# Kernel tuning notes

Measured on AMD Instinct MI355X. Metric: run time of the kernel, lower is better.

The kernel has to match this reference:

```python
import jax, jax.numpy as jnp
import numpy as np

NUM_STAGES = 8
NUM_CODEBOOKS = 1024  # 2**10
DATA_DIM = 256
T = 131072


def setup_inputs() -> dict:
    key = jax.random.key(0)
    k_x, k_cb = jax.random.split(key)
    input_data = jax.random.normal(k_x, (T, DATA_DIM), dtype=jnp.float32)
    # torch init: Uniform(-1/K, 1/K) per stage
    bound = 1.0 / NUM_CODEBOOKS
    codebooks = jax.random.uniform(
        k_cb, (NUM_STAGES, NUM_CODEBOOKS, DATA_DIM), dtype=jnp.float32,
        minval=-bound, maxval=bound)
    return {"input_data": input_data, "codebooks": codebooks}


def _hard_vq(residual, cb):
    dists = (jnp.sum(residual * residual, axis=1, keepdims=True)
             - 2.0 * (residual @ cb.T)
             + jnp.sum(cb * cb, axis=1)[None, :])
    idx = jnp.argmin(dists, axis=1)          # [T]
    q = cb[idx]                               # gather -> [T, D]
    return q, residual - q, idx


def reference(input_data, codebooks):
    # eval path: stage_map=None (mask of ones), train_mode=False
    residual = input_data
    recon = jnp.zeros_like(input_data)
    mses = []
    for i in range(codebooks.shape[0]):  # fixed small stage loop
        q, residual, _ = _hard_vq(residual, codebooks[i])
        recon = recon + q  # intermediate reconstruction = cumulative sum of q
        mses.append(jnp.mean((recon - input_data) ** 2))
    final_output = recon
    return final_output, jnp.stack(mses)
```

## Files before the change

kernel.cpp:

```cpp
#include <hip/hip_runtime.h>
#include <stdint.h>


#define T_ROWS   131072
#define DIM      256
#define NSTAGE   8
#define NCB      1024
#define WROWS    32
#define NWAVE    8
#define BLK_ROWS (NWAVE * WROWS)
#define NTHREADS (NWAVE * 64)
#define CHUNK_CW 32
#define NCHUNK   (NCB / CHUNK_CW)
#define CHUNK_BYTES (CHUNK_CW * 512)
#define NBUF     4

#define WS_CB_BYTES    (NSTAGE * NCB * 512)
#define WS_CNORM_OFF   WS_CB_BYTES
#define WS_CNORM_BYTES (NSTAGE * NCB * 4)
#define WS_MSE_OFF     (WS_CNORM_OFF + WS_CNORM_BYTES)
#define WS_IDX_OFF     (WS_MSE_OFF + 64)

typedef __attribute__((ext_vector_type(8)))  short  s16x8;
typedef __attribute__((ext_vector_type(8)))  __bf16 bf16x8;
typedef __attribute__((ext_vector_type(4)))  float  f32x4;
typedef __attribute__((ext_vector_type(16))) float  f32x16;

__device__ __forceinline__ unsigned short f2bf(float f) {
  union { float f; unsigned u; } v; v.f = f;
  unsigned r = v.u + 0x7FFFu + ((v.u >> 16) & 1u);
  return (unsigned short)(r >> 16);
}

__global__ void vq_prep(const float* __restrict__ CB, char* __restrict__ wscb,
                        float* __restrict__ cnorm) {
  const int tid = threadIdx.x;
  const int cwl = tid >> 5;
  const int j   = tid & 31;
  const int cw  = blockIdx.x * 8 + cwl;
  const int c   = cw & (NCB - 1);
  const float* src = CB + (size_t)cw * DIM + 8 * j;
  f32x4 a = *(const f32x4*)(src);
  f32x4 b = *(const f32x4*)(src + 4);
  s16x8 h;
#pragma unroll
  for (int e = 0; e < 4; ++e) { h[e] = (short)f2bf(a[e]); h[4 + e] = (short)f2bf(b[e]); }
  float sq = a[0]*a[0] + a[1]*a[1] + a[2]*a[2] + a[3]*a[3]
           + b[0]*b[0] + b[1]*b[1] + b[2]*b[2] + b[3]*b[3];
#pragma unroll
  for (int m = 1; m <= 16; m <<= 1) sq += __shfl_xor(sq, m);
  *(s16x8*)(wscb + (size_t)cw * 512 + ((16 * j) ^ ((c & 31) << 4))) = h;
  if (j == 0) cnorm[cw] = sq;
}

__global__ __launch_bounds__(NTHREADS, 4)
void vq_search(const float* __restrict__ X,
               const char* __restrict__ wscb, const float* __restrict__ cnorm,
               unsigned short* __restrict__ IDX, float* __restrict__ wsmse) {
  __shared__ __align__(16) char  lds_cb[NBUF][CHUNK_BYTES];
  __shared__ __align__(16) float lds_cn[NCB];
  __shared__ unsigned short lds_idx[BLK_ROWS];
  __shared__ float lds_n[BLK_ROWS];
  __shared__ float lds_msum[NWAVE];

  const int tid  = threadIdx.x;
  const int wave = tid >> 6;
  const int lane = tid & 63;
  const int c32  = lane & 31;
  const int hi   = lane >> 5;

  const int rowbase = blockIdx.x * BLK_ROWS + wave * WROWS;

  bf16x8 af[16];
  {
    const float* px = X + (size_t)(rowbase + c32) * DIM + 8 * hi;
    float s2 = 0.f;
#pragma unroll
    for (int s = 0; s < 16; ++s) {
      f32x4 a = *(const f32x4*)(px + 16 * s);
      f32x4 b = *(const f32x4*)(px + 16 * s + 4);
      bf16x8 tt;
#pragma unroll
      for (int e = 0; e < 4; ++e) {
        tt[e] = (__bf16)a[e]; tt[4 + e] = (__bf16)b[e];
        s2 += a[e] * a[e] + b[e] * b[e];
      }
      af[s] = tt;
    }
    float v = s2 + __shfl_xor(s2, 32);
    if (lane < 32) lds_n[wave * WROWS + c32] = v;
  }

  if (wave < 4)
    __builtin_amdgcn_global_load_lds(
        (const __attribute__((address_space(1))) char*)((const char*)cnorm + wave * 1024 + lane * 16),
        (__attribute__((address_space(3))) char*)((char*)lds_cn + wave * 1024),
        16, 0, 0);
#pragma unroll
  for (int ch = 0; ch < 3; ++ch)
#pragma unroll
    for (int i = 0; i < 2; ++i) {
      const int seg = (wave * 2 + i) * 1024;
      __builtin_amdgcn_global_load_lds(
          (const __attribute__((address_space(1))) char*)(wscb + (size_t)ch * CHUNK_BYTES + seg + lane * 16),
          (__attribute__((address_space(3))) char*)(&lds_cb[ch][0] + seg),
          16, 0, 0);
    }

  const int swz = c32 << 4;

#pragma unroll 1
  for (int st = 0; st < NSTAGE; ++st) {
    float mv[16];
#pragma unroll
    for (int r = 0; r < 16; ++r) mv[r] = -3.402823466e38f;

    const char* stage_cb = wscb + (size_t)st * NCB * 512;

#pragma unroll 1
    for (int ch = 0; ch < NCHUNK; ++ch) {
      const int cur = ch & (NBUF - 1);

      if (ch < NCHUNK - 2) {
        asm volatile("s_waitcnt vmcnt(4)" ::: "memory");
      } else if (ch == NCHUNK - 2) {
        asm volatile("s_waitcnt vmcnt(2)" ::: "memory");
      } else {
        asm volatile("s_waitcnt vmcnt(0)" ::: "memory");
      }
      __builtin_amdgcn_sched_barrier(0);
      __builtin_amdgcn_s_barrier();
      __builtin_amdgcn_sched_barrier(0);

      const float cnv = lds_cn[ch * CHUNK_CW + c32];
      f32x16 acc;
#pragma unroll
      for (int r = 0; r < 16; ++r) acc[r] = 0.f;

      const char* buf = &lds_cb[cur][0];
      __builtin_amdgcn_s_setprio(1);
#pragma unroll
      for (int s = 0; s < 16; ++s) {
        bf16x8 b = *(const bf16x8*)(buf + c32 * 512 + ((s * 32 + hi * 16) ^ swz));
        acc = __builtin_amdgcn_mfma_f32_32x32x16_bf16(af[s], b, acc, 0, 0, 0);
      }
      __builtin_amdgcn_s_setprio(0);

      if (ch + 3 < NCHUNK) {
        const char* src = stage_cb + (size_t)(ch + 3) * CHUNK_BYTES;
        char* dst = &lds_cb[(ch + 3) & (NBUF - 1)][0];
#pragma unroll
        for (int i = 0; i < 2; ++i) {
          const int seg = (wave * 2 + i) * 1024;
          __builtin_amdgcn_global_load_lds(
              (const __attribute__((address_space(1))) char*)(src + seg + lane * 16),
              (__attribute__((address_space(3))) char*)(dst + seg),
              16, 0, 0);
        }
      }

      const float cnh = 0.5f * cnv;
      const unsigned col = (unsigned)(ch * CHUNK_CW + c32);
#pragma unroll
      for (int r = 0; r < 16; ++r) {
        union { float f; unsigned u; } p;
        p.f = acc[r] - cnh;
        p.u = (p.u & 0xFFFFFC00u) | col;
        mv[r] = fmaxf(mv[r], p.f);
      }
    }

    float msum = 0.f;
#pragma unroll
    for (int r = 0; r < 16; ++r) {
      float v = mv[r];
#pragma unroll
      for (int m = 1; m <= 16; m <<= 1) v = fmaxf(v, __shfl_xor(v, m));
      union { float f; unsigned u; } w; w.f = v;
      const float vtrue = __builtin_bit_cast(float, w.u & 0xFFFFFC00u);
      const int   row   = (r & 3) + 8 * (r >> 2) + 4 * hi;
      const int   wrow  = wave * WROWS + row;
      const float n_new = lds_n[wrow] - 2.0f * vtrue;
      msum += n_new;
      if (c32 == 0) {
        lds_n[wrow]   = n_new;
        const int ix = (int)(w.u & 1023u);
        lds_idx[wrow] = (unsigned short)ix;
        IDX[st * T_ROWS + rowbase + row] = (unsigned short)ix;
      }
    }
    msum += __shfl_xor(msum, 32);
    if (lane == 0) lds_msum[wave] = msum;

    if (st != NSTAGE - 1) {
      const int idx = (int)lds_idx[wave * WROWS + c32];
      const char* q = stage_cb + (size_t)idx * 512;
      const int swzu = (idx & 31) << 4;
#pragma unroll
      for (int s = 0; s < 16; ++s) {
        bf16x8 qb = *(const bf16x8*)(q + ((s * 32 + hi * 16) ^ swzu));
        bf16x8 tt = af[s];
#pragma unroll
        for (int e = 0; e < 8; ++e)
          tt[e] = (__bf16)((float)tt[e] - (float)qb[e]);
        af[s] = tt;
      }
    }

    __builtin_amdgcn_sched_barrier(0);
    __builtin_amdgcn_s_barrier();
    __builtin_amdgcn_sched_barrier(0);

    if (wave == 0) {
      float v = (lane < NWAVE) ? lds_msum[lane] : 0.f;
#pragma unroll
      for (int m = 1; m < NWAVE; m <<= 1) v += __shfl_xor(v, m);
      if (lane == 0) atomicAdd(wsmse + st, v);
    }

    if (st != NSTAGE - 1) {
      const char* ncb = stage_cb + (size_t)NCB * 512;
      const char* ncn = (const char*)cnorm + (size_t)(st + 1) * NCB * 4;
      if (wave < 4)
        __builtin_amdgcn_global_load_lds(
            (const __attribute__((address_space(1))) char*)(ncn + wave * 1024 + lane * 16),
            (__attribute__((address_space(3))) char*)((char*)lds_cn + wave * 1024),
            16, 0, 0);
#pragma unroll
      for (int ch = 0; ch < 3; ++ch)
#pragma unroll
        for (int i = 0; i < 2; ++i) {
          const int seg = (wave * 2 + i) * 1024;
          __builtin_amdgcn_global_load_lds(
              (const __attribute__((address_space(1))) char*)(ncb + (size_t)ch * CHUNK_BYTES + seg + lane * 16),
              (__attribute__((address_space(3))) char*)(&lds_cb[ch][0] + seg),
              16, 0, 0);
        }
    }
  }
}

__global__ __launch_bounds__(256)
void vq_recon(const char* __restrict__ wscb, const unsigned short* __restrict__ IDX,
              float* __restrict__ OUT) {
  const int tid = threadIdx.x;
  const int row = blockIdx.x * (256 / 8) + (tid >> 3);
  const int g   = tid & 7;

  int idxs[NSTAGE];
#pragma unroll
  for (int st = 0; st < NSTAGE; ++st) idxs[st] = IDX[st * T_ROWS + row];

  float a[32];
#pragma unroll
  for (int d = 0; d < 32; ++d) a[d] = 0.f;

#pragma unroll
  for (int st = 0; st < NSTAGE; ++st) {
    const char* q = wscb + ((size_t)st * NCB + idxs[st]) * 512;
    const int swzu = (idxs[st] & 31) << 4;
#pragma unroll
    for (int k = 0; k < 4; ++k) {
      bf16x8 qb = *(const bf16x8*)(q + ((g * 64 + 16 * k) ^ swzu));
#pragma unroll
      for (int e = 0; e < 8; ++e) a[k * 8 + e] += (float)qb[e];
    }
  }

  float* po = OUT + (size_t)row * DIM + g * 32;
#pragma unroll
  for (int m = 0; m < 8; ++m) {
    f32x4 o = {a[4 * m], a[4 * m + 1], a[4 * m + 2], a[4 * m + 3]};
    *(f32x4*)(po + 4 * m) = o;
  }
}

__global__ void vq_fin(const float* __restrict__ wsmse, float* __restrict__ OUT) {
  const int i = threadIdx.x;
  if (i < NSTAGE) {
    OUT[(size_t)T_ROWS * DIM + i] = wsmse[i] * (1.0f / ((float)T_ROWS * (float)DIM));
  }
}

extern "C" void kernel_launch(void* const* d_in, const int* in_sizes, int n_in,
                              void* d_out, int out_size, void* d_ws, size_t ws_size,
                              hipStream_t stream) {
  (void)in_sizes; (void)n_in; (void)out_size; (void)ws_size;
  const float* X  = (const float*)d_in[0];
  const float* CB = (const float*)d_in[1];
  float* OUT = (float*)d_out;
  char*  wscb  = (char*)d_ws;
  float* cnorm = (float*)((char*)d_ws + WS_CNORM_OFF);
  float* wsmse = (float*)((char*)d_ws + WS_MSE_OFF);
  unsigned short* IDX = (unsigned short*)((char*)d_ws + WS_IDX_OFF);

  hipMemsetAsync(wsmse, 0, NSTAGE * sizeof(float), stream);
  hipLaunchKernelGGL(vq_prep, dim3((NSTAGE * NCB) / 8), dim3(256), 0, stream,
                     CB, wscb, cnorm);
  hipLaunchKernelGGL(vq_search, dim3(T_ROWS / BLK_ROWS), dim3(NTHREADS), 0, stream,
                     X, wscb, cnorm, IDX, wsmse);
  hipLaunchKernelGGL(vq_recon, dim3(T_ROWS / (256 / 8)), dim3(256), 0, stream,
                     wscb, IDX, OUT);
  hipLaunchKernelGGL(vq_fin, dim3(1), dim3(64), 0, stream, wsmse, OUT);
}
```

Baseline: 700.8 us.

## Give each wave four row tiles to reuse codebook LDS fragments across MFMAs

Each wave now processes 128 rows as four 32-row tiles with 4 waves per block, so each codebook fragment read from LDS feeds four MFMAs instead of one. This cuts LDS read traffic per MFMA and software-prefetches the next B fragment. It costs far more registers (four A tile sets, four accumulators and four max arrays), so launch bounds drop to one block per SM. Codebook streaming is now spread across fewer waves with more loads each, and fewer waves are available to hide latency.

```diff
diff --git a/kernel.cpp b/kernel.cpp
--- a/kernel.cpp
+++ b/kernel.cpp
@@ -6,8 +6,9 @@
 #define DIM      256
 #define NSTAGE   8
 #define NCB      1024
-#define WROWS    32
-#define NWAVE    8
+#define WROWS    128
+#define NTILE    4
+#define NWAVE    4
 #define BLK_ROWS (NWAVE * WROWS)
 #define NTHREADS (NWAVE * 64)
 #define CHUNK_CW 32
@@ -53,7 +54,7 @@
   if (j == 0) cnorm[cw] = sq;
 }
 
-__global__ __launch_bounds__(NTHREADS, 4)
+__global__ __launch_bounds__(NTHREADS, 1)
 void vq_search(const float* __restrict__ X,
                const char* __restrict__ wscb, const float* __restrict__ cnorm,
                unsigned short* __restrict__ IDX, float* __restrict__ wsmse) {
@@ -71,9 +72,10 @@
 
   const int rowbase = blockIdx.x * BLK_ROWS + wave * WROWS;
 
-  bf16x8 af[16];
-  {
-    const float* px = X + (size_t)(rowbase + c32) * DIM + 8 * hi;
+  bf16x8 af[NTILE][16];
+#pragma unroll
+  for (int t = 0; t < NTILE; ++t) {
+    const float* px = X + (size_t)(rowbase + t * 32 + c32) * DIM + 8 * hi;
     float s2 = 0.f;
 #pragma unroll
     for (int s = 0; s < 16; ++s) {
@@ -85,22 +87,21 @@
         tt[e] = (__bf16)a[e]; tt[4 + e] = (__bf16)b[e];
         s2 += a[e] * a[e] + b[e] * b[e];
       }
-      af[s] = tt;
+      af[t][s] = tt;
     }
     float v = s2 + __shfl_xor(s2, 32);
-    if (lane < 32) lds_n[wave * WROWS + c32] = v;
-  }
-
-  if (wave < 4)
-    __builtin_amdgcn_global_load_lds(
-        (const __attribute__((address_space(1))) char*)((const char*)cnorm + wave * 1024 + lane * 16),
-        (__attribute__((address_space(3))) char*)((char*)lds_cn + wave * 1024),
-        16, 0, 0);
+    if (lane < 32) lds_n[wave * WROWS + t * 32 + c32] = v;
+  }
+
+  __builtin_amdgcn_global_load_lds(
+      (const __attribute__((address_space(1))) char*)((const char*)cnorm + wave * 1024 + lane * 16),
+      (__attribute__((address_space(3))) char*)((char*)lds_cn + wave * 1024),
+      16, 0, 0);
 #pragma unroll
   for (int ch = 0; ch < 3; ++ch)
 #pragma unroll
-    for (int i = 0; i < 2; ++i) {
-      const int seg = (wave * 2 + i) * 1024;
+    for (int i = 0; i < 4; ++i) {
+      const int seg = (wave * 4 + i) * 1024;
       __builtin_amdgcn_global_load_lds(
           (const __attribute__((address_space(1))) char*)(wscb + (size_t)ch * CHUNK_BYTES + seg + lane * 16),
           (__attribute__((address_space(3))) char*)(&lds_cb[ch][0] + seg),
@@ -111,9 +112,11 @@
 
 #pragma unroll 1
   for (int st = 0; st < NSTAGE; ++st) {
-    float mv[16];
-#pragma unroll
-    for (int r = 0; r < 16; ++r) mv[r] = -3.402823466e38f;
+    float mv[NTILE][16];
+#pragma unroll
+    for (int t = 0; t < NTILE; ++t)
+#pragma unroll
+      for (int r = 0; r < 16; ++r) mv[t][r] = -3.402823466e38f;
 
     const char* stage_cb = wscb + (size_t)st * NCB * 512;
 
@@ -122,9 +125,9 @@
       const int cur = ch & (NBUF - 1);
 
       if (ch < NCHUNK - 2) {
+        asm volatile("s_waitcnt vmcnt(8)" ::: "memory");
+      } else if (ch == NCHUNK - 2) {
         asm volatile("s_waitcnt vmcnt(4)" ::: "memory");
-      } else if (ch == NCHUNK - 2) {
-        asm volatile("s_waitcnt vmcnt(2)" ::: "memory");
       } else {
         asm volatile("s_waitcnt vmcnt(0)" ::: "memory");
       }
@@ -133,16 +136,22 @@
       __builtin_amdgcn_sched_barrier(0);
 
       const float cnv = lds_cn[ch * CHUNK_CW + c32];
-      f32x16 acc;
-#pragma unroll
-      for (int r = 0; r < 16; ++r) acc[r] = 0.f;
-
-      const char* buf = &lds_cb[cur][0];
+      f32x16 acc0, acc1, acc2, acc3;
+#pragma unroll
+      for (int r = 0; r < 16; ++r) { acc0[r] = 0.f; acc1[r] = 0.f; acc2[r] = 0.f; acc3[r] = 0.f; }
+
+      const char* base = &lds_cb[cur][0] + c32 * 512;
       __builtin_amdgcn_s_setprio(1);
+      bf16x8 bcur = *(const bf16x8*)(base + ((hi * 16) ^ swz));
 #pragma unroll
       for (int s = 0; s < 16; ++s) {
-        bf16x8 b = *(const bf16x8*)(buf + c32 * 512 + ((s * 32 + hi * 16) ^ swz));
-        acc = __builtin_amdgcn_mfma_f32_32x32x16_bf16(af[s], b, acc, 0, 0, 0);
+        bf16x8 bnext;
+        if (s < 15) bnext = *(const bf16x8*)(base + (((s + 1) * 32 + hi * 16) ^ swz));
+        acc0 = __builtin_amdgcn_mfma_f32_32x32x16_bf16(af[0][s], bcur, acc0, 0, 0, 0);
+        acc1 = __builtin_amdgcn_mfma_f32_32x32x16_bf16(af[1][s], bcur, acc1, 0, 0, 0);
+        acc2 = __builtin_amdgcn_mfma_f32_32x32x16_bf16(af[2][s], bcur, acc2, 0, 0, 0);
+        acc3 = __builtin_amdgcn_mfma_f32_32x32x16_bf16(af[3][s], bcur, acc3, 0, 0, 0);
+        if (s < 15) bcur = bnext;
       }
       __builtin_amdgcn_s_setprio(0);
 
@@ -150,8 +159,8 @@
         const char* src = stage_cb + (size_t)(ch + 3) * CHUNK_BYTES;
         char* dst = &lds_cb[(ch + 3) & (NBUF - 1)][0];
 #pragma unroll
-        for (int i = 0; i < 2; ++i) {
-          const int seg = (wave * 2 + i) * 1024;
+        for (int i = 0; i < 4; ++i) {
+          const int seg = (wave * 4 + i) * 1024;
           __builtin_amdgcn_global_load_lds(
               (const __attribute__((address_space(1))) char*)(src + seg + lane * 16),
               (__attribute__((address_space(3))) char*)(dst + seg),
@@ -163,47 +172,57 @@
       const unsigned col = (unsigned)(ch * CHUNK_CW + c32);
 #pragma unroll
       for (int r = 0; r < 16; ++r) {
-        union { float f; unsigned u; } p;
-        p.f = acc[r] - cnh;
-        p.u = (p.u & 0xFFFFFC00u) | col;
-        mv[r] = fmaxf(mv[r], p.f);
+        union { float f; unsigned u; } p0, p1, p2, p3;
+        p0.f = acc0[r] - cnh; p0.u = (p0.u & 0xFFFFFC00u) | col;
+        p1.f = acc1[r] - cnh; p1.u = (p1.u & 0xFFFFFC00u) | col;
+        p2.f = acc2[r] - cnh; p2.u = (p2.u & 0xFFFFFC00u) | col;
+        p3.f = acc3[r] - cnh; p3.u = (p3.u & 0xFFFFFC00u) | col;
+        mv[0][r] = fmaxf(mv[0][r], p0.f);
+        mv[1][r] = fmaxf(mv[1][r], p1.f);
+        mv[2][r] = fmaxf(mv[2][r], p2.f);
+        mv[3][r] = fmaxf(mv[3][r], p3.f);
       }
     }
 
     float msum = 0.f;
 #pragma unroll
-    for (int r = 0; r < 16; ++r) {
-      float v = mv[r];
-#pragma unroll
-      for (int m = 1; m <= 16; m <<= 1) v = fmaxf(v, __shfl_xor(v, m));
-      union { float f; unsigned u; } w; w.f = v;
-      const float vtrue = __builtin_bit_cast(float, w.u & 0xFFFFFC00u);
-      const int   row   = (r & 3) + 8 * (r >> 2) + 4 * hi;
-      const int   wrow  = wave * WROWS + row;
-      const float n_new = lds_n[wrow] - 2.0f * vtrue;
-      msum += n_new;
-      if (c32 == 0) {
-        lds_n[wrow]   = n_new;
-        const int ix = (int)(w.u & 1023u);
-        lds_idx[wrow] = (unsigned short)ix;
-        IDX[st * T_ROWS + rowbase + row] = (unsigned short)ix;
-      }
-    }
+    for (int t = 0; t < NTILE; ++t)
+#pragma unroll
+      for (int r = 0; r < 16; ++r) {
+        float v = mv[t][r];
+#pragma unroll
+        for (int m = 1; m <= 16; m <<= 1) v = fmaxf(v, __shfl_xor(v, m));
+        union { float f; unsigned u; } w; w.f = v;
+        const float vtrue = __builtin_bit_cast(float, w.u & 0xFFFFFC00u);
+        const int   row   = t * 32 + (r & 3) + 8 * (r >> 2) + 4 * hi;
+        const int   wrow  = wave * WROWS + row;
+        const float n_new = lds_n[wrow] - 2.0f * vtrue;
+        msum += n_new;
+        if (c32 == 0) {
+          lds_n[wrow]   = n_new;
+          const int ix = (int)(w.u & 1023u);
+          lds_idx[wrow] = (unsigned short)ix;
+          IDX[st * T_ROWS + rowbase + row] = (unsigned short)ix;
+        }
+      }
     msum += __shfl_xor(msum, 32);
     if (lane == 0) lds_msum[wave] = msum;
 
     if (st != NSTAGE - 1) {
-      const int idx = (int)lds_idx[wave * WROWS + c32];
-      const char* q = stage_cb + (size_t)idx * 512;
-      const int swzu = (idx & 31) << 4;
-#pragma unroll
-      for (int s = 0; s < 16; ++s) {
-        bf16x8 qb = *(const bf16x8*)(q + ((s * 32 + hi * 16) ^ swzu));
-        bf16x8 tt = af[s];
-#pragma unroll
-        for (int e = 0; e < 8; ++e)
-          tt[e] = (__bf16)((float)tt[e] - (float)qb[e]);
-        af[s] = tt;
+#pragma unroll
+      for (int t = 0; t < NTILE; ++t) {
+        const int idx = (int)lds_idx[wave * WROWS + t * 32 + c32];
+        const char* q = stage_cb + (size_t)idx * 512;
+        const int swzu = (idx & 31) << 4;
+#pragma unroll
+        for (int s = 0; s < 16; ++s) {
+          bf16x8 qb = *(const bf16x8*)(q + ((s * 32 + hi * 16) ^ swzu));
+          bf16x8 tt = af[t][s];
+#pragma unroll
+          for (int e = 0; e < 8; ++e)
+            tt[e] = (__bf16)((float)tt[e] - (float)qb[e]);
+          af[t][s] = tt;
+        }
       }
     }
 
@@ -213,24 +232,23 @@
 
     if (wave == 0) {
       float v = (lane < NWAVE) ? lds_msum[lane] : 0.f;
-#pragma unroll
-      for (int m = 1; m < NWAVE; m <<= 1) v += __shfl_xor(v, m);
+      v += __shfl_xor(v, 1);
+      v += __shfl_xor(v, 2);
       if (lane == 0) atomicAdd(wsmse + st, v);
     }
 
     if (st != NSTAGE - 1) {
       const char* ncb = stage_cb + (size_t)NCB * 512;
       const char* ncn = (const char*)cnorm + (size_t)(st + 1) * NCB * 4;
-      if (wave < 4)
-        __builtin_amdgcn_global_load_lds(
-            (const __attribute__((address_space(1))) char*)(ncn + wave * 1024 + lane * 16),
-            (__attribute__((address_space(3))) char*)((char*)lds_cn + wave * 1024),
-            16, 0, 0);
+      __builtin_amdgcn_global_load_lds(
+          (const __attribute__((address_space(1))) char*)(ncn + wave * 1024 + lane * 16),
+          (__attribute__((address_space(3))) char*)((char*)lds_cn + wave * 1024),
+          16, 0, 0);
 #pragma unroll
       for (int ch = 0; ch < 3; ++ch)
 #pragma unroll
-        for (int i = 0; i < 2; ++i) {
-          const int seg = (wave * 2 + i) * 1024;
+        for (int i = 0; i < 4; ++i) {
+          const int seg = (wave * 4 + i) * 1024;
           __builtin_amdgcn_global_load_lds(
               (const __attribute__((address_space(1))) char*)(ncb + (size_t)ch * CHUNK_BYTES + seg + lane * 16),
               (__attribute__((address_space(3))) char*)(&lds_cb[ch][0] + seg),
```

Result: slower. 891.6 us (+27.2%).

## Pre-lay codebook in MFMA fragment order and pipeline chunks across stages

Applied to the files above, without the earlier changes.

The prep kernel now writes the bf16 codebook in MFMA B-fragment order, so LDS reads become contiguous per-lane loads with no XOR swizzle. The search kernel drops to 4 waves per block with a 3-buffer ring and a prefetch distance of two. The chunk index runs globally across stages, so the next stage's loads overlap the current stage's tail instead of being issued after the barrier. Codebook norms are read straight from global memory rather than staged in LDS, which adds global loads inside the inner loop and changes occupancy.

```diff
diff --git a/kernel.cpp b/kernel.cpp
--- a/kernel.cpp
+++ b/kernel.cpp
@@ -7,16 +7,16 @@
 #define NSTAGE   8
 #define NCB      1024
 #define WROWS    32
-#define NWAVE    8
+#define NWAVE    4
 #define BLK_ROWS (NWAVE * WROWS)
-#define NTHREADS (NWAVE * 64)
+#define NTHREADS 256
 #define CHUNK_CW 32
 #define NCHUNK   (NCB / CHUNK_CW)
+#define NGCH     (NSTAGE * NCHUNK)
 #define CHUNK_BYTES (CHUNK_CW * 512)
-#define NBUF     4
-
-#define WS_CB_BYTES    (NSTAGE * NCB * 512)
-#define WS_CNORM_OFF   WS_CB_BYTES
+
+#define WS_B_BYTES     (NSTAGE * NCB * 512)
+#define WS_CNORM_OFF   WS_B_BYTES
 #define WS_CNORM_BYTES (NSTAGE * NCB * 4)
 #define WS_MSE_OFF     (WS_CNORM_OFF + WS_CNORM_BYTES)
 #define WS_IDX_OFF     (WS_MSE_OFF + 64)
@@ -32,33 +32,46 @@
   return (unsigned short)(r >> 16);
 }
 
-__global__ void vq_prep(const float* __restrict__ CB, char* __restrict__ wscb,
+__global__ void vq_prep(const float* __restrict__ CB, char* __restrict__ wsb,
                         float* __restrict__ cnorm) {
   const int tid = threadIdx.x;
-  const int cwl = tid >> 5;
-  const int j   = tid & 31;
-  const int cw  = blockIdx.x * 8 + cwl;
-  const int c   = cw & (NCB - 1);
-  const float* src = CB + (size_t)cw * DIM + 8 * j;
-  f32x4 a = *(const f32x4*)(src);
-  f32x4 b = *(const f32x4*)(src + 4);
-  s16x8 h;
-#pragma unroll
-  for (int e = 0; e < 4; ++e) { h[e] = (short)f2bf(a[e]); h[4 + e] = (short)f2bf(b[e]); }
-  float sq = a[0]*a[0] + a[1]*a[1] + a[2]*a[2] + a[3]*a[3]
-           + b[0]*b[0] + b[1]*b[1] + b[2]*b[2] + b[3]*b[3];
-#pragma unroll
-  for (int m = 1; m <= 16; m <<= 1) sq += __shfl_xor(sq, m);
-  *(s16x8*)(wscb + (size_t)cw * 512 + ((16 * j) ^ ((c & 31) << 4))) = h;
-  if (j == 0) cnorm[cw] = sq;
-}
-
-__global__ __launch_bounds__(NTHREADS, 4)
+  const int b   = blockIdx.x;
+  {
+    const int g   = b >> 2;
+    const int s0  = (b & 3) * 4;
+    const int c32 = tid & 31;
+    const int sh  = tid >> 5;
+    const int s   = s0 + (sh >> 1);
+    const int hi  = sh & 1;
+    const int cw  = g * 32 + c32;
+    const float* src = CB + (size_t)cw * DIM + 16 * s + 8 * hi;
+    f32x4 a = *(const f32x4*)(src);
+    f32x4 c = *(const f32x4*)(src + 4);
+    s16x8 h;
+#pragma unroll
+    for (int e = 0; e < 4; ++e) { h[e] = (short)f2bf(a[e]); h[4 + e] = (short)f2bf(c[e]); }
+    *(s16x8*)(wsb + (size_t)g * 16384 + s * 1024 + hi * 512 + c32 * 16) = h;
+  }
+  {
+    const int cwl = tid >> 5;
+    const int j   = tid & 31;
+    const int cw  = b * 8 + cwl;
+    const float* src = CB + (size_t)cw * DIM + 8 * j;
+    f32x4 a = *(const f32x4*)(src);
+    f32x4 c = *(const f32x4*)(src + 4);
+    float sq = a[0]*a[0] + a[1]*a[1] + a[2]*a[2] + a[3]*a[3]
+             + c[0]*c[0] + c[1]*c[1] + c[2]*c[2] + c[3]*c[3];
+#pragma unroll
+    for (int m = 1; m <= 16; m <<= 1) sq += __shfl_xor(sq, m);
+    if (j == 0) cnorm[cw] = sq;
+  }
+}
+
+__global__ __launch_bounds__(NTHREADS, 3)
 void vq_search(const float* __restrict__ X,
-               const char* __restrict__ wscb, const float* __restrict__ cnorm,
+               const char* __restrict__ wsb, const float* __restrict__ cnorm,
                unsigned short* __restrict__ IDX, float* __restrict__ wsmse) {
-  __shared__ __align__(16) char  lds_cb[NBUF][CHUNK_BYTES];
-  __shared__ __align__(16) float lds_cn[NCB];
+  __shared__ __align__(16) char  lds_cb[3][CHUNK_BYTES];
   __shared__ unsigned short lds_idx[BLK_ROWS];
   __shared__ float lds_n[BLK_ROWS];
   __shared__ float lds_msum[NWAVE];
@@ -91,23 +104,16 @@
     if (lane < 32) lds_n[wave * WROWS + c32] = v;
   }
 
-  if (wave < 4)
-    __builtin_amdgcn_global_load_lds(
-        (const __attribute__((address_space(1))) char*)((const char*)cnorm + wave * 1024 + lane * 16),
-        (__attribute__((address_space(3))) char*)((char*)lds_cn + wave * 1024),
-        16, 0, 0);
-#pragma unroll
-  for (int ch = 0; ch < 3; ++ch)
-#pragma unroll
-    for (int i = 0; i < 2; ++i) {
-      const int seg = (wave * 2 + i) * 1024;
+#pragma unroll
+  for (int g = 0; g < 2; ++g)
+#pragma unroll
+    for (int i = 0; i < 4; ++i) {
+      const int seg = (wave * 4 + i) * 1024;
       __builtin_amdgcn_global_load_lds(
-          (const __attribute__((address_space(1))) char*)(wscb + (size_t)ch * CHUNK_BYTES + seg + lane * 16),
-          (__attribute__((address_space(3))) char*)(&lds_cb[ch][0] + seg),
+          (const __attribute__((address_space(1))) char*)(wsb + (size_t)g * CHUNK_BYTES + seg + lane * 16),
+          (__attribute__((address_space(3))) char*)(&lds_cb[g][0] + seg),
           16, 0, 0);
     }
-
-  const int swz = c32 << 4;
 
 #pragma unroll 1
   for (int st = 0; st < NSTAGE; ++st) {
@@ -115,16 +121,12 @@
 #pragma unroll
     for (int r = 0; r < 16; ++r) mv[r] = -3.402823466e38f;
 
-    const char* stage_cb = wscb + (size_t)st * NCB * 512;
-
 #pragma unroll 1
     for (int ch = 0; ch < NCHUNK; ++ch) {
-      const int cur = ch & (NBUF - 1);
-
-      if (ch < NCHUNK - 2) {
+      const int gf = st * NCHUNK + ch;
+
+      if (gf < NGCH - 2) {
         asm volatile("s_waitcnt vmcnt(4)" ::: "memory");
-      } else if (ch == NCHUNK - 2) {
-        asm volatile("s_waitcnt vmcnt(2)" ::: "memory");
       } else {
         asm volatile("s_waitcnt vmcnt(0)" ::: "memory");
       }
@@ -132,30 +134,34 @@
       __builtin_amdgcn_s_barrier();
       __builtin_amdgcn_sched_barrier(0);
 
-      const float cnv = lds_cn[ch * CHUNK_CW + c32];
+      const float cnv = cnorm[gf * CHUNK_CW + c32];
+
       f32x16 acc;
 #pragma unroll
       for (int r = 0; r < 16; ++r) acc[r] = 0.f;
 
-      const char* buf = &lds_cb[cur][0];
+      const char* buf = &lds_cb[gf % 3][0] + lane * 16;
       __builtin_amdgcn_s_setprio(1);
 #pragma unroll
       for (int s = 0; s < 16; ++s) {
-        bf16x8 b = *(const bf16x8*)(buf + c32 * 512 + ((s * 32 + hi * 16) ^ swz));
+        bf16x8 b = *(const bf16x8*)(buf + s * 1024);
         acc = __builtin_amdgcn_mfma_f32_32x32x16_bf16(af[s], b, acc, 0, 0, 0);
       }
       __builtin_amdgcn_s_setprio(0);
 
-      if (ch + 3 < NCHUNK) {
-        const char* src = stage_cb + (size_t)(ch + 3) * CHUNK_BYTES;
-        char* dst = &lds_cb[(ch + 3) & (NBUF - 1)][0];
-#pragma unroll
-        for (int i = 0; i < 2; ++i) {
-          const int seg = (wave * 2 + i) * 1024;
-          __builtin_amdgcn_global_load_lds(
-              (const __attribute__((address_space(1))) char*)(src + seg + lane * 16),
-              (__attribute__((address_space(3))) char*)(dst + seg),
-              16, 0, 0);
+      {
+        const int gt = gf + 2;
+        if (gt < NGCH) {
+          const char* src = wsb + (size_t)gt * CHUNK_BYTES;
+          char* dst = &lds_cb[gt % 3][0];
+#pragma unroll
+          for (int i = 0; i < 4; ++i) {
+            const int seg = (wave * 4 + i) * 1024;
+            __builtin_amdgcn_global_load_lds(
+                (const __attribute__((address_space(1))) char*)(src + seg + lane * 16),
+                (__attribute__((address_space(3))) char*)(dst + seg),
+                16, 0, 0);
+          }
         }
       }
 
@@ -194,11 +200,11 @@
 
     if (st != NSTAGE - 1) {
       const int idx = (int)lds_idx[wave * WROWS + c32];
-      const char* q = stage_cb + (size_t)idx * 512;
-      const int swzu = (idx & 31) << 4;
+      const char* q = wsb + (size_t)st * NCB * 512
+                    + (size_t)(idx >> 5) * 16384 + hi * 512 + (idx & 31) * 16;
 #pragma unroll
       for (int s = 0; s < 16; ++s) {
-        bf16x8 qb = *(const bf16x8*)(q + ((s * 32 + hi * 16) ^ swzu));
+        bf16x8 qb = *(const bf16x8*)(q + s * 1024);
         bf16x8 tt = af[s];
 #pragma unroll
         for (int e = 0; e < 8; ++e)
@@ -207,41 +213,19 @@
       }
     }
 
-    __builtin_amdgcn_sched_barrier(0);
     __builtin_amdgcn_s_barrier();
-    __builtin_amdgcn_sched_barrier(0);
 
     if (wave == 0) {
       float v = (lane < NWAVE) ? lds_msum[lane] : 0.f;
-#pragma unroll
-      for (int m = 1; m < NWAVE; m <<= 1) v += __shfl_xor(v, m);
+      v += __shfl_xor(v, 1);
+      v += __shfl_xor(v, 2);
       if (lane == 0) atomicAdd(wsmse + st, v);
     }
-
-    if (st != NSTAGE - 1) {
-      const char* ncb = stage_cb + (size_t)NCB * 512;
-      const char* ncn = (const char*)cnorm + (size_t)(st + 1) * NCB * 4;
-      if (wave < 4)
-        __builtin_amdgcn_global_load_lds(
-            (const __attribute__((address_space(1))) char*)(ncn + wave * 1024 + lane * 16),
-            (__attribute__((address_space(3))) char*)((char*)lds_cn + wave * 1024),
-            16, 0, 0);
-#pragma unroll
-      for (int ch = 0; ch < 3; ++ch)
-#pragma unroll
-        for (int i = 0; i < 2; ++i) {
-          const int seg = (wave * 2 + i) * 1024;
-          __builtin_amdgcn_global_load_lds(
-              (const __attribute__((address_space(1))) char*)(ncb + (size_t)ch * CHUNK_BYTES + seg + lane * 16),
-              (__attribute__((address_space(3))) char*)(&lds_cb[ch][0] + seg),
-              16, 0, 0);
-        }
-    }
   }
 }
 
 __global__ __launch_bounds__(256)
-void vq_recon(const char* __restrict__ wscb, const unsigned short* __restrict__ IDX,
+void vq_recon(const char* __restrict__ wsb, const unsigned short* __restrict__ IDX,
               float* __restrict__ OUT) {
   const int tid = threadIdx.x;
   const int row = blockIdx.x * (256 / 8) + (tid >> 3);
@@ -257,11 +241,13 @@
 
 #pragma unroll
   for (int st = 0; st < NSTAGE; ++st) {
-    const char* q = wscb + ((size_t)st * NCB + idxs[st]) * 512;
-    const int swzu = (idxs[st] & 31) << 4;
+    const char* q = wsb + (size_t)st * NCB * 512
+                  + (size_t)(idxs[st] >> 5) * 16384 + (idxs[st] & 31) * 16;
 #pragma unroll
     for (int k = 0; k < 4; ++k) {
-      bf16x8 qb = *(const bf16x8*)(q + ((g * 64 + 16 * k) ^ swzu));
+      const int s  = 2 * g + (k >> 1);
+      const int h2 = (k & 1);
+      bf16x8 qb = *(const bf16x8*)(q + s * 1024 + h2 * 512);
 #pragma unroll
       for (int e = 0; e < 8; ++e) a[k * 8 + e] += (float)qb[e];
     }
@@ -289,17 +275,17 @@
   const float* X  = (const float*)d_in[0];
   const float* CB = (const float*)d_in[1];
   float* OUT = (float*)d_out;
-  char*  wscb  = (char*)d_ws;
+  char*  wsb   = (char*)d_ws;
   float* cnorm = (float*)((char*)d_ws + WS_CNORM_OFF);
   float* wsmse = (float*)((char*)d_ws + WS_MSE_OFF);
   unsigned short* IDX = (unsigned short*)((char*)d_ws + WS_IDX_OFF);
 
   hipMemsetAsync(wsmse, 0, NSTAGE * sizeof(float), stream);
-  hipLaunchKernelGGL(vq_prep, dim3((NSTAGE * NCB) / 8), dim3(256), 0, stream,
-                     CB, wscb, cnorm);
+  hipLaunchKernelGGL(vq_prep, dim3(1024), dim3(256), 0, stream,
+                     CB, wsb, cnorm);
   hipLaunchKernelGGL(vq_search, dim3(T_ROWS / BLK_ROWS), dim3(NTHREADS), 0, stream,
-                     X, wscb, cnorm, IDX, wsmse);
+                     X, wsb, cnorm, IDX, wsmse);
   hipLaunchKernelGGL(vq_recon, dim3(T_ROWS / (256 / 8)), dim3(256), 0, stream,
-                     wscb, IDX, OUT);
+                     wsb, IDX, OUT);
   hipLaunchKernelGGL(vq_fin, dim3(1), dim3(64), 0, stream, wsmse, OUT);
 }
```

Measured after the change: 885.3 us. 26.3% more time.
